# Kernel optimization log

Measured on AMD Instinct MI355X. Metric: run time of the kernel, lower is better.

## Reference

```python
import jax, jax.numpy as jnp
import numpy as np

O, I = 4096, 4096          # out_features, in_features
N = 8192                   # tokens (batch*seq)
ROW_BS, COL_BS = 1, 4      # block sparsity granularity
ZP_OUT = 0                 # output zero point (int)
QMIN, QMAX = -128.0, 127.0 # qint8 range


def setup_inputs() -> dict:
    key = jax.random.key(0)
    k1, k2, k3, k4 = jax.random.split(key, 4)
    # dequantized fp32 activations
    x = jax.random.normal(k1, (N, I), dtype=jnp.float32)
    # int8 weight values (zero point 0), stored as float32 integers in [-127,127]
    w_q = jnp.round(jnp.clip(jax.random.normal(k2, (O, I), dtype=jnp.float32) * 40.0, QMIN + 1, QMAX))
    bias = jax.random.normal(k3, (O,), dtype=jnp.float32) * 0.1
    block_mask = jax.random.randint(k4, (O // ROW_BS, I // COL_BS), 0, 2, dtype=jnp.int32)
    w_scale = jnp.float32(0.01)   # per-tensor weight scale, weight zp == 0
    out_scale = jnp.float32(0.05) # activation (output) quant scale
    return {"x": x, "w_q": w_q, "bias": bias, "w_scale": w_scale,
            "out_scale": out_scale, "block_mask": block_mask}


def reference(x, w_q, bias, w_scale, out_scale, block_mask):
    # expand block mask to element mask [O, I]
    m = jnp.repeat(jnp.repeat(block_mask, ROW_BS, axis=0), COL_BS, axis=1).astype(w_q.dtype)
    w_eff = w_q * m                                  # masked int8 weight values
    # dequantized GEMM: (x @ W^T) * w_scale + bias
    y = jnp.einsum('ni,oi->no', x, w_eff) * w_scale + bias  # [N, O]
    # quantize output to qint8 (scale=out_scale, zp=ZP_OUT), return dequantized repr
    q = jnp.clip(jnp.round(y / out_scale) + ZP_OUT, QMIN, QMAX)
    return (q - ZP_OUT) * out_scale
```

## Files before the change

kernel.cpp:

```cpp
#include <hip/hip_runtime.h>


#define M_TOK 8192
#define O_FEAT 4096
#define K_FEAT 4096

#define BM 256
#define BN 256
#define BK 64
#define NT (K_FEAT / BK)

#define S_BUF 32768
#define S_MAT 16384
#define S_KH  8192

using f16x8 = __attribute__((ext_vector_type(8))) _Float16;
using f32x4 = __attribute__((ext_vector_type(4))) float;

#define BAR()    asm volatile("s_barrier" ::: "memory")
#define VMCNT(n) asm volatile("s_waitcnt vmcnt(" #n ")" ::: "memory")
#define MFMA16(a, b, c) __builtin_amdgcn_mfma_f32_16x16x32_f16((a), (b), (c), 0, 0, 0)

__global__ __launch_bounds__(256) void cvt_x_kernel(const float* __restrict__ x,
                                                    _Float16* __restrict__ xf) {
    size_t i = ((size_t)blockIdx.x * 256 + threadIdx.x) * 8;
    float4 v0 = *reinterpret_cast<const float4*>(x + i);
    float4 v1 = *reinterpret_cast<const float4*>(x + i + 4);
    f16x8 h;
    h[0] = (_Float16)v0.x; h[1] = (_Float16)v0.y;
    h[2] = (_Float16)v0.z; h[3] = (_Float16)v0.w;
    h[4] = (_Float16)v1.x; h[5] = (_Float16)v1.y;
    h[6] = (_Float16)v1.z; h[7] = (_Float16)v1.w;
    *reinterpret_cast<f16x8*>(xf + i) = h;
}

__global__ __launch_bounds__(256) void cvt_w_kernel(const float* __restrict__ wq,
                                                    const int* __restrict__ mask,
                                                    _Float16* __restrict__ wf) {
    size_t i = ((size_t)blockIdx.x * 256 + threadIdx.x) * 8;
    float4 v0 = *reinterpret_cast<const float4*>(wq + i);
    float4 v1 = *reinterpret_cast<const float4*>(wq + i + 4);
    int2 mv = *reinterpret_cast<const int2*>(mask + i / 4);
    float m0 = mv.x ? 1.0f : 0.0f;
    float m1 = mv.y ? 1.0f : 0.0f;
    f16x8 h;
    h[0] = (_Float16)(v0.x * m0); h[1] = (_Float16)(v0.y * m0);
    h[2] = (_Float16)(v0.z * m0); h[3] = (_Float16)(v0.w * m0);
    h[4] = (_Float16)(v1.x * m1); h[5] = (_Float16)(v1.y * m1);
    h[6] = (_Float16)(v1.z * m1); h[7] = (_Float16)(v1.w * m1);
    *reinterpret_cast<f16x8*>(wf + i) = h;
}

__global__ __launch_bounds__(512, 2) void gemm_kernel(const _Float16* __restrict__ A,
                                                      const _Float16* __restrict__ B,
                                                      const float* __restrict__ bias,
                                                      const float* __restrict__ wsp,
                                                      const float* __restrict__ osp,
                                                      float* __restrict__ C) {
    __shared__ __align__(16) _Float16 smem[2][2][2][BM * 32];
    _Float16* sm = &smem[0][0][0][0];

    const int tid  = threadIdx.x;
    const int lane = tid & 63;
    const int w    = tid >> 6;
    const int wm   = w >> 2;
    const int wn   = w & 3;
    const int lr   = lane & 15;
    const int kq   = lane >> 4;

    const int bm = blockIdx.x >> 4;
    const int bn = blockIdx.x & 15;

    const int sr0  = w * 32 + (lane >> 2);
    const int csrc = ((lane & 3) ^ ((lane >> 3) & 3)) * 8;
    const size_t J1 = (size_t)16 * K_FEAT;

    const _Float16* pA0 = A + (size_t)(bm * BM + sr0) * K_FEAT + csrc;
    const _Float16* pA1 = pA0 + 32;
    const _Float16* pB0 = B + (size_t)(bn * BN + sr0) * K_FEAT + csrc;
    const _Float16* pB1 = pB0 + 32;

    const int dst0 = (w * 128 + lane) * 8;
    const int dst1 = dst0 + 64 * 8;

    auto stg = [&](const _Float16* src, _Float16* dstp) {
        __builtin_amdgcn_global_load_lds(
            (const __attribute__((address_space(1))) void*)(const void*)src,
            (__attribute__((address_space(3))) void*)(void*)dstp, 16, 0, 0);
    };

    int offA[4], offB[4];
#pragma unroll
    for (int m = 0; m < 4; ++m) {
        const int r = wm * 128 + m * 16 + lr;
        offA[m] = r * 32 + ((kq ^ ((r >> 1) & 3)) << 3);
    }
#pragma unroll
    for (int n = 0; n < 4; ++n) {
        const int r = wn * 64 + n * 16 + lr;
        offB[n] = r * 32 + ((kq ^ ((r >> 1) & 3)) << 3);
    }
    auto rd = [&](const _Float16* sbuf, int off, int immE) -> f16x8 {
        return *reinterpret_cast<const f16x8*>(sbuf + off + immE);
    };

    f32x4 acc[8][4] = {};
    f16x8 a0[4], a1[4], b0v[4], b1v[4];

    stg(pA0, sm + dst0);                    stg(pA0 + J1, sm + dst1);
    stg(pB0, sm + S_MAT + dst0);            stg(pB0 + J1, sm + S_MAT + dst1);
    VMCNT(0);
    BAR();
#pragma unroll
    for (int m = 0; m < 4; ++m) a0[m] = rd(sm, offA[m], 0);
#pragma unroll
    for (int n = 0; n < 4; ++n) b0v[n] = rd(sm, offB[n], S_MAT);
    stg(pA1, sm + S_KH + dst0);             stg(pA1 + J1, sm + S_KH + dst1);
    stg(pB1, sm + S_MAT + S_KH + dst0);     stg(pB1 + J1, sm + S_MAT + S_KH + dst1);
    pA0 += BK; pA1 += BK; pB0 += BK; pB1 += BK;

    for (int s = 0; s < NT; ++s) {
        const _Float16* sb = sm + ((s & 1) ? S_BUF : 0);
        _Float16*       sn = sm + ((s & 1) ? 0 : S_BUF);
        const bool more = (s + 1 < NT);

#pragma unroll
        for (int m = 0; m < 4; ++m) a1[m] = rd(sb, offA[m], 2048);
        if (more) { stg(pA0, sn + dst0); stg(pA0 + J1, sn + dst1); }
        BAR();
        __builtin_amdgcn_s_setprio(1);
#pragma unroll
        for (int m = 0; m < 4; ++m)
#pragma unroll
            for (int n = 0; n < 4; ++n)
                acc[m][n] = MFMA16(a0[m], b0v[n], acc[m][n]);
        __builtin_amdgcn_s_setprio(0);
        if (s == NT - 1) { VMCNT(0); } else { VMCNT(2); }
        BAR();

#pragma unroll
        for (int m = 0; m < 4; ++m) a0[m] = rd(sb, offA[m], S_KH);
#pragma unroll
        for (int n = 0; n < 4; ++n) b1v[n] = rd(sb, offB[n], S_MAT + S_KH);
        if (more) { stg(pB0, sn + S_MAT + dst0); stg(pB0 + J1, sn + S_MAT + dst1); }
        BAR();
        __builtin_amdgcn_s_setprio(1);
#pragma unroll
        for (int m = 0; m < 4; ++m)
#pragma unroll
            for (int n = 0; n < 4; ++n)
                acc[4 + m][n] = MFMA16(a1[m], b0v[n], acc[4 + m][n]);
        __builtin_amdgcn_s_setprio(0);

#pragma unroll
        for (int m = 0; m < 4; ++m) a1[m] = rd(sb, offA[m], S_KH + 2048);
        if (more) { stg(pA1, sn + S_KH + dst0); stg(pA1 + J1, sn + S_KH + dst1); }
        BAR();
        __builtin_amdgcn_s_setprio(1);
#pragma unroll
        for (int m = 0; m < 4; ++m)
#pragma unroll
            for (int n = 0; n < 4; ++n)
                acc[m][n] = MFMA16(a0[m], b1v[n], acc[m][n]);
        __builtin_amdgcn_s_setprio(0);
        if (more) { VMCNT(2); BAR(); }

        if (more) {
#pragma unroll
            for (int m = 0; m < 4; ++m) a0[m] = rd(sn, offA[m], 0);
#pragma unroll
            for (int n = 0; n < 4; ++n) b0v[n] = rd(sn, offB[n], S_MAT);
            stg(pB1, sn + S_MAT + S_KH + dst0); stg(pB1 + J1, sn + S_MAT + S_KH + dst1);
            pA0 += BK; pA1 += BK; pB0 += BK; pB1 += BK;
        }
        BAR();
        __builtin_amdgcn_s_setprio(1);
#pragma unroll
        for (int m = 0; m < 4; ++m)
#pragma unroll
            for (int n = 0; n < 4; ++n)
                acc[4 + m][n] = MFMA16(a1[m], b1v[n], acc[4 + m][n]);
        __builtin_amdgcn_s_setprio(0);
    }

    const float wscale = wsp[0];
    const float oscale = osp[0];
    const int row0 = bm * BM + wm * 128;
    const int col0 = bn * BN + wn * 64;
#pragma unroll
    for (int n = 0; n < 4; ++n) {
        const int col = col0 + n * 16 + lr;
        const float bc = bias[col];
#pragma unroll
        for (int m = 0; m < 8; ++m) {
#pragma unroll
            for (int j = 0; j < 4; ++j) {
                const int row = row0 + m * 16 + kq * 4 + j;
                float y = acc[m][n][j] * wscale + bc;
                float q = rintf(y / oscale);
                q = fminf(fmaxf(q, -128.0f), 127.0f);
                C[(size_t)row * O_FEAT + col] = q * oscale;
            }
        }
    }
}

extern "C" void kernel_launch(void* const* d_in, const int* in_sizes, int n_in,
                              void* d_out, int out_size, void* d_ws, size_t ws_size,
                              hipStream_t stream) {
    const float* x        = (const float*)d_in[0];
    const float* wq       = (const float*)d_in[1];
    const float* bias     = (const float*)d_in[2];
    const float* w_scale  = (const float*)d_in[3];
    const float* out_scale= (const float*)d_in[4];
    const int*   mask     = (const int*)d_in[5];
    float* out = (float*)d_out;

    _Float16* xf = (_Float16*)d_ws;
    _Float16* wf = (_Float16*)((char*)d_ws + (size_t)M_TOK * K_FEAT * 2);

    cvt_x_kernel<<<(M_TOK * (size_t)K_FEAT) / 8 / 256, 256, 0, stream>>>(x, xf);
    cvt_w_kernel<<<(O_FEAT * (size_t)K_FEAT) / 8 / 256, 256, 0, stream>>>(wq, mask, wf);

    gemm_kernel<<<dim3((M_TOK / BM) * (O_FEAT / BN)), 512, 0, stream>>>(
        xf, wf, bias, w_scale, out_scale, out);
}
```

Baseline: 296.2 us.

## Prefetch two K-tiles ahead in GEMM and merge conversion kernels

Restructures the GEMM main loop so global-to-LDS loads run two K-steps ahead, writing into the buffer just consumed rather than the next one. The B-fragment LDS reads are split across phases, and explicit lgkmcnt waits plus sched_barriers replace some of the vmcnt-based waits. The two fp32-to-fp16 conversion kernels are fused into one launch with a block-index split, saving a launch. The deeper prefetch hides more global latency, at the cost of tighter correctness reasoning around buffer reuse and barriers.

```diff
diff --git a/kernel.cpp b/kernel.cpp
--- a/kernel.cpp
+++ b/kernel.cpp
@@ -18,37 +18,43 @@
 using f32x4 = __attribute__((ext_vector_type(4))) float;
 
 #define BAR()    asm volatile("s_barrier" ::: "memory")
+#define LGKM0()  asm volatile("s_waitcnt lgkmcnt(0)" ::: "memory")
 #define VMCNT(n) asm volatile("s_waitcnt vmcnt(" #n ")" ::: "memory")
+#define SB0()    __builtin_amdgcn_sched_barrier(0)
 #define MFMA16(a, b, c) __builtin_amdgcn_mfma_f32_16x16x32_f16((a), (b), (c), 0, 0, 0)
 
-__global__ __launch_bounds__(256) void cvt_x_kernel(const float* __restrict__ x,
-                                                    _Float16* __restrict__ xf) {
-    size_t i = ((size_t)blockIdx.x * 256 + threadIdx.x) * 8;
-    float4 v0 = *reinterpret_cast<const float4*>(x + i);
-    float4 v1 = *reinterpret_cast<const float4*>(x + i + 4);
-    f16x8 h;
-    h[0] = (_Float16)v0.x; h[1] = (_Float16)v0.y;
-    h[2] = (_Float16)v0.z; h[3] = (_Float16)v0.w;
-    h[4] = (_Float16)v1.x; h[5] = (_Float16)v1.y;
-    h[6] = (_Float16)v1.z; h[7] = (_Float16)v1.w;
-    *reinterpret_cast<f16x8*>(xf + i) = h;
-}
-
-__global__ __launch_bounds__(256) void cvt_w_kernel(const float* __restrict__ wq,
-                                                    const int* __restrict__ mask,
-                                                    _Float16* __restrict__ wf) {
-    size_t i = ((size_t)blockIdx.x * 256 + threadIdx.x) * 8;
-    float4 v0 = *reinterpret_cast<const float4*>(wq + i);
-    float4 v1 = *reinterpret_cast<const float4*>(wq + i + 4);
-    int2 mv = *reinterpret_cast<const int2*>(mask + i / 4);
-    float m0 = mv.x ? 1.0f : 0.0f;
-    float m1 = mv.y ? 1.0f : 0.0f;
-    f16x8 h;
-    h[0] = (_Float16)(v0.x * m0); h[1] = (_Float16)(v0.y * m0);
-    h[2] = (_Float16)(v0.z * m0); h[3] = (_Float16)(v0.w * m0);
-    h[4] = (_Float16)(v1.x * m1); h[5] = (_Float16)(v1.y * m1);
-    h[6] = (_Float16)(v1.z * m1); h[7] = (_Float16)(v1.w * m1);
-    *reinterpret_cast<f16x8*>(wf + i) = h;
+#define NXBLK (M_TOK * K_FEAT / 8 / 256)
+
+__global__ __launch_bounds__(256) void cvt_kernel(const float* __restrict__ x,
+                                                  const float* __restrict__ wq,
+                                                  const int* __restrict__ mask,
+                                                  _Float16* __restrict__ xf,
+                                                  _Float16* __restrict__ wf) {
+    const int b = blockIdx.x;
+    if (b < NXBLK) {
+        size_t i = ((size_t)b * 256 + threadIdx.x) * 8;
+        float4 v0 = *reinterpret_cast<const float4*>(x + i);
+        float4 v1 = *reinterpret_cast<const float4*>(x + i + 4);
+        f16x8 h;
+        h[0] = (_Float16)v0.x; h[1] = (_Float16)v0.y;
+        h[2] = (_Float16)v0.z; h[3] = (_Float16)v0.w;
+        h[4] = (_Float16)v1.x; h[5] = (_Float16)v1.y;
+        h[6] = (_Float16)v1.z; h[7] = (_Float16)v1.w;
+        *reinterpret_cast<f16x8*>(xf + i) = h;
+    } else {
+        size_t i = ((size_t)(b - NXBLK) * 256 + threadIdx.x) * 8;
+        float4 v0 = *reinterpret_cast<const float4*>(wq + i);
+        float4 v1 = *reinterpret_cast<const float4*>(wq + i + 4);
+        int2 mv = *reinterpret_cast<const int2*>(mask + i / 4);
+        float m0 = mv.x ? 1.0f : 0.0f;
+        float m1 = mv.y ? 1.0f : 0.0f;
+        f16x8 h;
+        h[0] = (_Float16)(v0.x * m0); h[1] = (_Float16)(v0.y * m0);
+        h[2] = (_Float16)(v0.z * m0); h[3] = (_Float16)(v0.w * m0);
+        h[4] = (_Float16)(v1.x * m1); h[5] = (_Float16)(v1.y * m1);
+        h[6] = (_Float16)(v1.z * m1); h[7] = (_Float16)(v1.w * m1);
+        *reinterpret_cast<f16x8*>(wf + i) = h;
+    }
 }
 
 __global__ __launch_bounds__(512, 2) void gemm_kernel(const _Float16* __restrict__ A,
@@ -83,10 +89,11 @@
     const int dst0 = (w * 128 + lane) * 8;
     const int dst1 = dst0 + 64 * 8;
 
-    auto stg = [&](const _Float16* src, _Float16* dstp) {
+    auto stg = [&](const _Float16* src, const _Float16* dstp) {
         __builtin_amdgcn_global_load_lds(
             (const __attribute__((address_space(1))) void*)(const void*)src,
-            (__attribute__((address_space(3))) void*)(void*)dstp, 16, 0, 0);
+            (__attribute__((address_space(3))) void*)(void*)(_Float16*)(uintptr_t)dstp,
+            16, 0, 0);
     };
 
     int offA[4], offB[4];
@@ -107,27 +114,37 @@
     f32x4 acc[8][4] = {};
     f16x8 a0[4], a1[4], b0v[4], b1v[4];
 
-    stg(pA0, sm + dst0);                    stg(pA0 + J1, sm + dst1);
-    stg(pB0, sm + S_MAT + dst0);            stg(pB0 + J1, sm + S_MAT + dst1);
-    VMCNT(0);
+    stg(pA0, sm + dst0);                 stg(pA0 + J1, sm + dst1);
+    stg(pB0, sm + S_MAT + dst0);         stg(pB0 + J1, sm + S_MAT + dst1);
+    stg(pA1, sm + S_KH + dst0);          stg(pA1 + J1, sm + S_KH + dst1);
+    stg(pB1, sm + S_MAT + S_KH + dst0);  stg(pB1 + J1, sm + S_MAT + S_KH + dst1);
+    pA0 += BK; pA1 += BK; pB0 += BK; pB1 += BK;
+    stg(pA0, sm + S_BUF + dst0);                 stg(pA0 + J1, sm + S_BUF + dst1);
+    stg(pB0, sm + S_BUF + S_MAT + dst0);         stg(pB0 + J1, sm + S_BUF + S_MAT + dst1);
+    stg(pA1, sm + S_BUF + S_KH + dst0);          stg(pA1 + J1, sm + S_BUF + S_KH + dst1);
+    stg(pB1, sm + S_BUF + S_MAT + S_KH + dst0);  stg(pB1 + J1, sm + S_BUF + S_MAT + S_KH + dst1);
+    pA0 += BK; pA1 += BK; pB0 += BK; pB1 += BK;
+    VMCNT(8);
     BAR();
 #pragma unroll
     for (int m = 0; m < 4; ++m) a0[m] = rd(sm, offA[m], 0);
 #pragma unroll
     for (int n = 0; n < 4; ++n) b0v[n] = rd(sm, offB[n], S_MAT);
-    stg(pA1, sm + S_KH + dst0);             stg(pA1 + J1, sm + S_KH + dst1);
-    stg(pB1, sm + S_MAT + S_KH + dst0);     stg(pB1 + J1, sm + S_MAT + S_KH + dst1);
-    pA0 += BK; pA1 += BK; pB0 += BK; pB1 += BK;
+    LGKM0();
+    BAR();
 
     for (int s = 0; s < NT; ++s) {
         const _Float16* sb = sm + ((s & 1) ? S_BUF : 0);
-        _Float16*       sn = sm + ((s & 1) ? 0 : S_BUF);
+        const _Float16* sn = sm + ((s & 1) ? 0 : S_BUF);
         const bool more = (s + 1 < NT);
+        const bool stg_ok = (s + 2 < NT);
 
 #pragma unroll
         for (int m = 0; m < 4; ++m) a1[m] = rd(sb, offA[m], 2048);
-        if (more) { stg(pA0, sn + dst0); stg(pA0 + J1, sn + dst1); }
-        BAR();
+        b1v[0] = rd(sb, offB[0], S_MAT + S_KH);
+        b1v[1] = rd(sb, offB[1], S_MAT + S_KH);
+        if (stg_ok) { stg(pB0, sb + S_MAT + dst0); stg(pB0 + J1, sb + S_MAT + dst1); }
+        SB0();
         __builtin_amdgcn_s_setprio(1);
 #pragma unroll
         for (int m = 0; m < 4; ++m)
@@ -135,15 +152,15 @@
             for (int n = 0; n < 4; ++n)
                 acc[m][n] = MFMA16(a0[m], b0v[n], acc[m][n]);
         __builtin_amdgcn_s_setprio(0);
-        if (s == NT - 1) { VMCNT(0); } else { VMCNT(2); }
+        SB0(); LGKM0();
         BAR();
 
 #pragma unroll
         for (int m = 0; m < 4; ++m) a0[m] = rd(sb, offA[m], S_KH);
-#pragma unroll
-        for (int n = 0; n < 4; ++n) b1v[n] = rd(sb, offB[n], S_MAT + S_KH);
-        if (more) { stg(pB0, sn + S_MAT + dst0); stg(pB0 + J1, sn + S_MAT + dst1); }
-        BAR();
+        b1v[2] = rd(sb, offB[2], S_MAT + S_KH);
+        b1v[3] = rd(sb, offB[3], S_MAT + S_KH);
+        if (stg_ok) { stg(pA0, sb + dst0); stg(pA0 + J1, sb + dst1); }
+        SB0();
         __builtin_amdgcn_s_setprio(1);
 #pragma unroll
         for (int m = 0; m < 4; ++m)
@@ -151,11 +168,18 @@
             for (int n = 0; n < 4; ++n)
                 acc[4 + m][n] = MFMA16(a1[m], b0v[n], acc[4 + m][n]);
         __builtin_amdgcn_s_setprio(0);
+        SB0(); LGKM0();
+        if (s >= NT - 2) { VMCNT(0); } else { VMCNT(4); }
+        BAR();
 
 #pragma unroll
         for (int m = 0; m < 4; ++m) a1[m] = rd(sb, offA[m], S_KH + 2048);
-        if (more) { stg(pA1, sn + S_KH + dst0); stg(pA1 + J1, sn + S_KH + dst1); }
-        BAR();
+        if (more) {
+            b0v[0] = rd(sn, offB[0], S_MAT);
+            b0v[1] = rd(sn, offB[1], S_MAT);
+        }
+        if (stg_ok) { stg(pB1, sb + S_MAT + S_KH + dst0); stg(pB1 + J1, sb + S_MAT + S_KH + dst1); }
+        SB0();
         __builtin_amdgcn_s_setprio(1);
 #pragma unroll
         for (int m = 0; m < 4; ++m)
@@ -163,17 +187,19 @@
             for (int n = 0; n < 4; ++n)
                 acc[m][n] = MFMA16(a0[m], b1v[n], acc[m][n]);
         __builtin_amdgcn_s_setprio(0);
-        if (more) { VMCNT(2); BAR(); }
+        SB0(); LGKM0();
+        BAR();
 
         if (more) {
 #pragma unroll
             for (int m = 0; m < 4; ++m) a0[m] = rd(sn, offA[m], 0);
-#pragma unroll
-            for (int n = 0; n < 4; ++n) b0v[n] = rd(sn, offB[n], S_MAT);
-            stg(pB1, sn + S_MAT + S_KH + dst0); stg(pB1 + J1, sn + S_MAT + S_KH + dst1);
-            pA0 += BK; pA1 += BK; pB0 += BK; pB1 += BK;
-        }
-        BAR();
+            b0v[2] = rd(sn, offB[2], S_MAT);
+            b0v[3] = rd(sn, offB[3], S_MAT);
+        }
+        if (stg_ok) {
+            stg(pA1, sb + S_KH + dst0); stg(pA1 + J1, sb + S_KH + dst1);
+        }
+        SB0();
         __builtin_amdgcn_s_setprio(1);
 #pragma unroll
         for (int m = 0; m < 4; ++m)
@@ -181,6 +207,10 @@
             for (int n = 0; n < 4; ++n)
                 acc[4 + m][n] = MFMA16(a1[m], b1v[n], acc[4 + m][n]);
         __builtin_amdgcn_s_setprio(0);
+        SB0(); LGKM0();
+        BAR();
+
+        pA0 += BK; pA1 += BK; pB0 += BK; pB1 += BK;
     }
 
     const float wscale = wsp[0];
@@ -219,8 +249,7 @@
     _Float16* xf = (_Float16*)d_ws;
     _Float16* wf = (_Float16*)((char*)d_ws + (size_t)M_TOK * K_FEAT * 2);
 
-    cvt_x_kernel<<<(M_TOK * (size_t)K_FEAT) / 8 / 256, 256, 0, stream>>>(x, xf);
-    cvt_w_kernel<<<(O_FEAT * (size_t)K_FEAT) / 8 / 256, 256, 0, stream>>>(wq, mask, wf);
+    cvt_kernel<<<NXBLK + (O_FEAT * K_FEAT / 8 / 256), 256, 0, stream>>>(x, wq, mask, xf, wf);
 
     gemm_kernel<<<dim3((M_TOK / BM) * (O_FEAT / BN)), 512, 0, stream>>>(
         xf, wf, bias, w_scale, out_scale, out);
```

New measurement: 293.4 us. Within noise of the previous version (-0.9%).

## Load B fragments directly to registers, fuse conversion kernels, remap block order

Applied to the files above, without the earlier changes.

The GEMM stops staging the weight tile through LDS. Each lane now loads its B fragments straight from global memory into registers, which halves the LDS footprint and drops the B staging and LDS reads, and the A pipeline is reworked to prefetch two stages with explicit vmcnt and lgkmcnt waits and sched barriers. The two fp32-to-fp16 conversion kernels are merged into one launch, and the block index mapping is changed so consecutive blocks share a B column tile. The risks are B global loads that are not coalesced, per-wave redundancy in B traffic, and fragile hand-counted waitcnt values.

```diff
diff --git a/kernel.cpp b/kernel.cpp
--- a/kernel.cpp
+++ b/kernel.cpp
@@ -10,45 +10,50 @@
 #define BK 64
 #define NT (K_FEAT / BK)
 
-#define S_BUF 32768
-#define S_MAT 16384
+#define S_BUF 16384
 #define S_KH  8192
 
 using f16x8 = __attribute__((ext_vector_type(8))) _Float16;
 using f32x4 = __attribute__((ext_vector_type(4))) float;
 
 #define BAR()    asm volatile("s_barrier" ::: "memory")
+#define LGKM0()  asm volatile("s_waitcnt lgkmcnt(0)" ::: "memory")
 #define VMCNT(n) asm volatile("s_waitcnt vmcnt(" #n ")" ::: "memory")
+#define SB0()    __builtin_amdgcn_sched_barrier(0)
 #define MFMA16(a, b, c) __builtin_amdgcn_mfma_f32_16x16x32_f16((a), (b), (c), 0, 0, 0)
 
-__global__ __launch_bounds__(256) void cvt_x_kernel(const float* __restrict__ x,
-                                                    _Float16* __restrict__ xf) {
-    size_t i = ((size_t)blockIdx.x * 256 + threadIdx.x) * 8;
-    float4 v0 = *reinterpret_cast<const float4*>(x + i);
-    float4 v1 = *reinterpret_cast<const float4*>(x + i + 4);
-    f16x8 h;
-    h[0] = (_Float16)v0.x; h[1] = (_Float16)v0.y;
-    h[2] = (_Float16)v0.z; h[3] = (_Float16)v0.w;
-    h[4] = (_Float16)v1.x; h[5] = (_Float16)v1.y;
-    h[6] = (_Float16)v1.z; h[7] = (_Float16)v1.w;
-    *reinterpret_cast<f16x8*>(xf + i) = h;
-}
-
-__global__ __launch_bounds__(256) void cvt_w_kernel(const float* __restrict__ wq,
-                                                    const int* __restrict__ mask,
-                                                    _Float16* __restrict__ wf) {
-    size_t i = ((size_t)blockIdx.x * 256 + threadIdx.x) * 8;
-    float4 v0 = *reinterpret_cast<const float4*>(wq + i);
-    float4 v1 = *reinterpret_cast<const float4*>(wq + i + 4);
-    int2 mv = *reinterpret_cast<const int2*>(mask + i / 4);
-    float m0 = mv.x ? 1.0f : 0.0f;
-    float m1 = mv.y ? 1.0f : 0.0f;
-    f16x8 h;
-    h[0] = (_Float16)(v0.x * m0); h[1] = (_Float16)(v0.y * m0);
-    h[2] = (_Float16)(v0.z * m0); h[3] = (_Float16)(v0.w * m0);
-    h[4] = (_Float16)(v1.x * m1); h[5] = (_Float16)(v1.y * m1);
-    h[6] = (_Float16)(v1.z * m1); h[7] = (_Float16)(v1.w * m1);
-    *reinterpret_cast<f16x8*>(wf + i) = h;
+#define NXBLK (M_TOK * K_FEAT / 8 / 256)
+
+__global__ __launch_bounds__(256) void cvt_kernel(const float* __restrict__ x,
+                                                  const float* __restrict__ wq,
+                                                  const int* __restrict__ mask,
+                                                  _Float16* __restrict__ xf,
+                                                  _Float16* __restrict__ wf) {
+    const int b = blockIdx.x;
+    if (b < NXBLK) {
+        size_t i = ((size_t)b * 256 + threadIdx.x) * 8;
+        float4 v0 = *reinterpret_cast<const float4*>(x + i);
+        float4 v1 = *reinterpret_cast<const float4*>(x + i + 4);
+        f16x8 h;
+        h[0] = (_Float16)v0.x; h[1] = (_Float16)v0.y;
+        h[2] = (_Float16)v0.z; h[3] = (_Float16)v0.w;
+        h[4] = (_Float16)v1.x; h[5] = (_Float16)v1.y;
+        h[6] = (_Float16)v1.z; h[7] = (_Float16)v1.w;
+        *reinterpret_cast<f16x8*>(xf + i) = h;
+    } else {
+        size_t i = ((size_t)(b - NXBLK) * 256 + threadIdx.x) * 8;
+        float4 v0 = *reinterpret_cast<const float4*>(wq + i);
+        float4 v1 = *reinterpret_cast<const float4*>(wq + i + 4);
+        int2 mv = *reinterpret_cast<const int2*>(mask + i / 4);
+        float m0 = mv.x ? 1.0f : 0.0f;
+        float m1 = mv.y ? 1.0f : 0.0f;
+        f16x8 h;
+        h[0] = (_Float16)(v0.x * m0); h[1] = (_Float16)(v0.y * m0);
+        h[2] = (_Float16)(v0.z * m0); h[3] = (_Float16)(v0.w * m0);
+        h[4] = (_Float16)(v1.x * m1); h[5] = (_Float16)(v1.y * m1);
+        h[6] = (_Float16)(v1.z * m1); h[7] = (_Float16)(v1.w * m1);
+        *reinterpret_cast<f16x8*>(wf + i) = h;
+    }
 }
 
 __global__ __launch_bounds__(512, 2) void gemm_kernel(const _Float16* __restrict__ A,
@@ -57,8 +62,8 @@
                                                       const float* __restrict__ wsp,
                                                       const float* __restrict__ osp,
                                                       float* __restrict__ C) {
-    __shared__ __align__(16) _Float16 smem[2][2][2][BM * 32];
-    _Float16* sm = &smem[0][0][0][0];
+    __shared__ __align__(16) _Float16 smem[2][2][BM * 32];
+    _Float16* sm = &smem[0][0][0];
 
     const int tid  = threadIdx.x;
     const int lane = tid & 63;
@@ -68,8 +73,8 @@
     const int lr   = lane & 15;
     const int kq   = lane >> 4;
 
-    const int bm = blockIdx.x >> 4;
-    const int bn = blockIdx.x & 15;
+    const int bn = blockIdx.x >> 5;
+    const int bm = blockIdx.x & 31;
 
     const int sr0  = w * 32 + (lane >> 2);
     const int csrc = ((lane & 3) ^ ((lane >> 3) & 3)) * 8;
@@ -77,8 +82,6 @@
 
     const _Float16* pA0 = A + (size_t)(bm * BM + sr0) * K_FEAT + csrc;
     const _Float16* pA1 = pA0 + 32;
-    const _Float16* pB0 = B + (size_t)(bn * BN + sr0) * K_FEAT + csrc;
-    const _Float16* pB1 = pB0 + 32;
 
     const int dst0 = (w * 128 + lane) * 8;
     const int dst1 = dst0 + 64 * 8;
@@ -89,98 +92,108 @@
             (__attribute__((address_space(3))) void*)(void*)dstp, 16, 0, 0);
     };
 
-    int offA[4], offB[4];
+    int offA[4];
 #pragma unroll
     for (int m = 0; m < 4; ++m) {
         const int r = wm * 128 + m * 16 + lr;
         offA[m] = r * 32 + ((kq ^ ((r >> 1) & 3)) << 3);
     }
-#pragma unroll
-    for (int n = 0; n < 4; ++n) {
-        const int r = wn * 64 + n * 16 + lr;
-        offB[n] = r * 32 + ((kq ^ ((r >> 1) & 3)) << 3);
-    }
-    auto rd = [&](const _Float16* sbuf, int off, int immE) -> f16x8 {
-        return *reinterpret_cast<const f16x8*>(sbuf + off + immE);
-    };
+
+    const _Float16* pBv[4];
+#pragma unroll
+    for (int nf = 0; nf < 4; ++nf)
+        pBv[nf] = B + (size_t)(bn * BN + wn * 64 + nf * 16 + lr) * K_FEAT + kq * 8;
 
     f32x4 acc[8][4] = {};
-    f16x8 a0[4], a1[4], b0v[4], b1v[4];
-
-    stg(pA0, sm + dst0);                    stg(pA0 + J1, sm + dst1);
-    stg(pB0, sm + S_MAT + dst0);            stg(pB0 + J1, sm + S_MAT + dst1);
+    f16x8 a0[4], a1[4], bv0[4], bv1[4];
+
+    stg(pA0, sm + dst0);                        stg(pA0 + J1, sm + dst1);
+    stg(pA1, sm + S_KH + dst0);                 stg(pA1 + J1, sm + S_KH + dst1);
+    stg(pA0 + BK, sm + S_BUF + dst0);           stg(pA0 + BK + J1, sm + S_BUF + dst1);
+    stg(pA1 + BK, sm + S_BUF + S_KH + dst0);    stg(pA1 + BK + J1, sm + S_BUF + S_KH + dst1);
+#pragma unroll
+    for (int nf = 0; nf < 4; ++nf) bv0[nf] = *reinterpret_cast<const f16x8*>(pBv[nf]);
     VMCNT(0);
     BAR();
 #pragma unroll
-    for (int m = 0; m < 4; ++m) a0[m] = rd(sm, offA[m], 0);
-#pragma unroll
-    for (int n = 0; n < 4; ++n) b0v[n] = rd(sm, offB[n], S_MAT);
-    stg(pA1, sm + S_KH + dst0);             stg(pA1 + J1, sm + S_KH + dst1);
-    stg(pB1, sm + S_MAT + S_KH + dst0);     stg(pB1 + J1, sm + S_MAT + S_KH + dst1);
-    pA0 += BK; pA1 += BK; pB0 += BK; pB1 += BK;
-
-    for (int s = 0; s < NT; ++s) {
-        const _Float16* sb = sm + ((s & 1) ? S_BUF : 0);
-        _Float16*       sn = sm + ((s & 1) ? 0 : S_BUF);
-        const bool more = (s + 1 < NT);
-
-#pragma unroll
-        for (int m = 0; m < 4; ++m) a1[m] = rd(sb, offA[m], 2048);
-        if (more) { stg(pA0, sn + dst0); stg(pA0 + J1, sn + dst1); }
+    for (int m = 0; m < 4; ++m) a0[m] = *reinterpret_cast<const f16x8*>(sm + offA[m]);
+    pA0 += 2 * BK; pA1 += 2 * BK;
+
+    for (int t = 0; t < NT; ++t) {
+        _Float16* bufp = sm + ((t & 1) ? S_BUF : 0);
+        const _Float16* bufn = sm + ((t & 1) ? 0 : S_BUF);
+        const bool more = (t + 1 < NT);
+        const bool stg_ok = (t + 2 < NT);
+
+#pragma unroll
+        for (int m = 0; m < 4; ++m)
+            a1[m] = *reinterpret_cast<const f16x8*>(bufp + offA[m] + 2048);
+#pragma unroll
+        for (int nf = 0; nf < 4; ++nf)
+            bv1[nf] = *reinterpret_cast<const f16x8*>(pBv[nf] + 32);
+        if (t == NT - 1) { VMCNT(4); } else { VMCNT(6); }
+        SB0();
+        __builtin_amdgcn_s_setprio(1);
+#pragma unroll
+        for (int m = 0; m < 4; ++m)
+#pragma unroll
+            for (int n = 0; n < 4; ++n)
+                acc[m][n] = MFMA16(a0[m], bv0[n], acc[m][n]);
+        __builtin_amdgcn_s_setprio(0);
+        LGKM0();
         BAR();
-        __builtin_amdgcn_s_setprio(1);
-#pragma unroll
-        for (int m = 0; m < 4; ++m)
-#pragma unroll
-            for (int n = 0; n < 4; ++n)
-                acc[m][n] = MFMA16(a0[m], b0v[n], acc[m][n]);
-        __builtin_amdgcn_s_setprio(0);
-        if (s == NT - 1) { VMCNT(0); } else { VMCNT(2); }
+
+#pragma unroll
+        for (int m = 0; m < 4; ++m)
+            a0[m] = *reinterpret_cast<const f16x8*>(bufp + offA[m] + S_KH);
+        if (stg_ok) { stg(pA0, bufp + dst0); stg(pA0 + J1, bufp + dst1); }
+        SB0();
+        __builtin_amdgcn_s_setprio(1);
+#pragma unroll
+        for (int m = 0; m < 4; ++m)
+#pragma unroll
+            for (int n = 0; n < 4; ++n)
+                acc[4 + m][n] = MFMA16(a1[m], bv0[n], acc[4 + m][n]);
+        __builtin_amdgcn_s_setprio(0);
+
+#pragma unroll
+        for (int m = 0; m < 4; ++m)
+            a1[m] = *reinterpret_cast<const f16x8*>(bufp + offA[m] + S_KH + 2048);
+        if (more) {
+#pragma unroll
+            for (int nf = 0; nf < 4; ++nf)
+                bv0[nf] = *reinterpret_cast<const f16x8*>(pBv[nf] + 64);
+        }
+        if (stg_ok) { VMCNT(6); } else if (t == NT - 2) { VMCNT(4); } else { VMCNT(0); }
+        SB0();
+        __builtin_amdgcn_s_setprio(1);
+#pragma unroll
+        for (int m = 0; m < 4; ++m)
+#pragma unroll
+            for (int n = 0; n < 4; ++n)
+                acc[m][n] = MFMA16(a0[m], bv1[n], acc[m][n]);
+        __builtin_amdgcn_s_setprio(0);
+        LGKM0();
         BAR();
 
-#pragma unroll
-        for (int m = 0; m < 4; ++m) a0[m] = rd(sb, offA[m], S_KH);
-#pragma unroll
-        for (int n = 0; n < 4; ++n) b1v[n] = rd(sb, offB[n], S_MAT + S_KH);
-        if (more) { stg(pB0, sn + S_MAT + dst0); stg(pB0 + J1, sn + S_MAT + dst1); }
-        BAR();
-        __builtin_amdgcn_s_setprio(1);
-#pragma unroll
-        for (int m = 0; m < 4; ++m)
-#pragma unroll
-            for (int n = 0; n < 4; ++n)
-                acc[4 + m][n] = MFMA16(a1[m], b0v[n], acc[4 + m][n]);
-        __builtin_amdgcn_s_setprio(0);
-
-#pragma unroll
-        for (int m = 0; m < 4; ++m) a1[m] = rd(sb, offA[m], S_KH + 2048);
-        if (more) { stg(pA1, sn + S_KH + dst0); stg(pA1 + J1, sn + S_KH + dst1); }
-        BAR();
-        __builtin_amdgcn_s_setprio(1);
-#pragma unroll
-        for (int m = 0; m < 4; ++m)
-#pragma unroll
-            for (int n = 0; n < 4; ++n)
-                acc[m][n] = MFMA16(a0[m], b1v[n], acc[m][n]);
-        __builtin_amdgcn_s_setprio(0);
-        if (more) { VMCNT(2); BAR(); }
-
         if (more) {
 #pragma unroll
-            for (int m = 0; m < 4; ++m) a0[m] = rd(sn, offA[m], 0);
-#pragma unroll
-            for (int n = 0; n < 4; ++n) b0v[n] = rd(sn, offB[n], S_MAT);
-            stg(pB1, sn + S_MAT + S_KH + dst0); stg(pB1 + J1, sn + S_MAT + S_KH + dst1);
-            pA0 += BK; pA1 += BK; pB0 += BK; pB1 += BK;
+            for (int m = 0; m < 4; ++m)
+                a0[m] = *reinterpret_cast<const f16x8*>(bufn + offA[m]);
         }
-        BAR();
-        __builtin_amdgcn_s_setprio(1);
-#pragma unroll
-        for (int m = 0; m < 4; ++m)
-#pragma unroll
-            for (int n = 0; n < 4; ++n)
-                acc[4 + m][n] = MFMA16(a1[m], b1v[n], acc[4 + m][n]);
-        __builtin_amdgcn_s_setprio(0);
+        if (stg_ok) { stg(pA1, bufp + S_KH + dst0); stg(pA1 + J1, bufp + S_KH + dst1); }
+        SB0();
+        __builtin_amdgcn_s_setprio(1);
+#pragma unroll
+        for (int m = 0; m < 4; ++m)
+#pragma unroll
+            for (int n = 0; n < 4; ++n)
+                acc[4 + m][n] = MFMA16(a1[m], bv1[n], acc[4 + m][n]);
+        __builtin_amdgcn_s_setprio(0);
+
+        pA0 += BK; pA1 += BK;
+#pragma unroll
+        for (int nf = 0; nf < 4; ++nf) pBv[nf] += BK;
     }
 
     const float wscale = wsp[0];
@@ -219,8 +232,7 @@
     _Float16* xf = (_Float16*)d_ws;
     _Float16* wf = (_Float16*)((char*)d_ws + (size_t)M_TOK * K_FEAT * 2);
 
-    cvt_x_kernel<<<(M_TOK * (size_t)K_FEAT) / 8 / 256, 256, 0, stream>>>(x, xf);
-    cvt_w_kernel<<<(O_FEAT * (size_t)K_FEAT) / 8 / 256, 256, 0, stream>>>(wq, mask, wf);
+    cvt_kernel<<<NXBLK + (O_FEAT * K_FEAT / 8 / 256), 256, 0, stream>>>(x, wq, mask, xf, wf);
 
     gemm_kernel<<<dim3((M_TOK / BM) * (O_FEAT / BN)), 512, 0, stream>>>(
         xf, wf, bias, w_scale, out_scale, out);
```

Result: slower. 426.1 us (+43.9%).
